# Kernel tuning notes

Measured on AMD Instinct MI355X. Metric: run time of the kernel, lower is better.

## Reference

```python
import jax, jax.numpy as jnp
import numpy as np

# Static config matching init_kwargs
COUT, CIN, K = 64, 64, 3
PAD = K // 2  # padding=1


def setup_inputs() -> dict:
    key = jax.random.key(0)
    k1, k2, k3 = jax.random.split(key, 3)
    B, H, W, FH, FW, SC = 2, 256, 256, 16, 16, 128
    hyper_params = COUT * CIN * K * K  # 36864
    x = jax.random.normal(k1, (B, CIN, H, W), jnp.float32)
    s = jax.random.normal(k2, (B, SC, FH, FW), jnp.float32)
    s2w = jax.random.normal(k3, (hyper_params, SC), jnp.float32) * 0.02
    return {"x": x, "s": s, "s2w": s2w}


def reference(x, s, s2w):
    """HyperPatchConv2d forward: per-patch dynamically generated 3x3 conv.

    x:   [b, c, h, w]   input feature map
    s:   [b, sc, fh, fw] hypernetwork signal (one vector per patch)
    s2w: [P, sc]         signal2weights 1x1 conv (P = out*cin*k*k)
    """
    b, c, h, w = x.shape
    fh, fw = s.shape[-2:]
    ph, pw = h // fh, w // fw          # patch size
    kh, kw = ph + 2 * PAD, pw + 2 * PAD  # unfold window (patch + halo)

    # signal2weights: 1x1 conv -> per-patch flattened conv weight
    wflat = jnp.einsum('pc,bcfg->bfgp', s2w, s)            # [b,fh,fw,P]
    Wdyn = wflat.reshape(b, fh, fw, COUT, CIN, K, K)        # per-patch conv kernels

    # reflect-pad then unfold into overlapping (kh,kw) patches, stride (ph,pw)
    xp = jnp.pad(x, ((0, 0), (0, 0), (PAD, PAD), (PAD, PAD)), mode='reflect')
    idx_h = (jnp.arange(fh) * ph)[:, None] + jnp.arange(kh)[None, :]  # [fh,kh]
    idx_w = (jnp.arange(fw) * pw)[:, None] + jnp.arange(kw)[None, :]  # [fw,kw]
    patches = xp[:, :, idx_h][:, :, :, :, idx_w]            # [b,c,fh,kh,fw,kw]

    # extract KxK sliding windows inside each patch (valid conv, stride 1)
    wi = jnp.arange(ph)[:, None] + jnp.arange(K)[None, :]   # [ph,K]
    wj = jnp.arange(pw)[:, None] + jnp.arange(K)[None, :]   # [pw,K]
    win = patches[:, :, :, wi]                              # [b,c,fh,ph,K,fw,kw]
    win = win[:, :, :, :, :, :, wj]                         # [b,c,fh,ph,K,fw,pw,K]
    win = win.transpose(0, 2, 5, 1, 3, 4, 6, 7)             # [b,fh,fw,c,ph,K,pw,K]

    # per-patch dynamic conv
    out = jnp.einsum('bfgocij,bfgcpiqj->bfgopq', Wdyn, win)  # [b,fh,fw,o,ph,pw]

    # fold: non-overlapping reassembly (stride == patch size)
    return out.transpose(0, 3, 1, 4, 2, 5).reshape(b, COUT, h, w)
```

## Files before the change

### kernel.cpp

```cpp
#include <hip/hip_runtime.h>
#include <hip/hip_bf16.h>


#define C_OUT 64
#define C_IN  64
#define P_TOTAL 36864
#define N_PATCH 512
#define WSTR 72
#define CSTR2 136

typedef __bf16 bf16x8 __attribute__((ext_vector_type(8)));
typedef float  f32x4  __attribute__((ext_vector_type(4)));

__device__ __forceinline__ unsigned short f2bf(float f) {
  unsigned int u = __float_as_uint(f);
  u += 0x7fffu + ((u >> 16) & 1u);
  return (unsigned short)(u >> 16);
}
__device__ __forceinline__ unsigned int pack2(float a, float b) {
  return (unsigned int)f2bf(a) | ((unsigned int)f2bf(b) << 16);
}
__device__ __forceinline__ void gll16(const void* g, void* l) {
  __builtin_amdgcn_global_load_lds(
      (const __attribute__((address_space(1))) void*)g,
      (__attribute__((address_space(3))) void*)l, 16, 0, 0);
}

__global__ __launch_bounds__(256) void prep_ws(
    const float* __restrict__ s, const float* __restrict__ s2w,
    unsigned short* __restrict__ sTg, unsigned short* __restrict__ s2wP) {
  const int bid = blockIdx.x;
  const int t = threadIdx.x;

  if (bid < 32) {
    const int sb = bid >> 4;
    const int g = bid & 15;
    float v[8];
    #pragma unroll
    for (int e = 0; e < 8; ++e)
      v[e] = s[((size_t)(sb * 128 + g * 8 + e)) * 256 + t];
    uint4 o;
    o.x = pack2(v[0], v[1]); o.y = pack2(v[2], v[3]);
    o.z = pack2(v[4], v[5]); o.w = pack2(v[6], v[7]);
    const int ntile = sb * 2 + (t >> 7);
    const int slot = (t & 127) ^ (g & 7);
    *(uint4*)(sTg + ((size_t)(ntile * 2048 + g * 128 + slot)) * 8) = o;
    return;
  }

  const int b3 = bid - 32;
  const int m = b3 * 64 + (t >> 2);
  const int q = t & 3;
  const int j = m & 7;
  const int lane6 = (m >> 3) & 63;
  const int fragidx = m >> 9;
  const int tap = fragidx >> 3;
  const int ksH = (fragidx >> 2) & 1;
  const int mtH = fragidx & 3;
  const int co = mtH * 16 + (lane6 & 15);
  const int ci = ksH * 32 + (lane6 >> 4) * 8 + j;
  const int p = co * 576 + ci * 9 + tap;
  const float* src = s2w + (size_t)p * 128 + q * 32;
  const int mtile = m >> 7;
  const int r128 = m & 127;
  #pragma unroll
  for (int gg = 0; gg < 4; ++gg) {
    const int g = q * 4 + gg;
    const float4 v0 = *(const float4*)(src + gg * 8);
    const float4 v1 = *(const float4*)(src + gg * 8 + 4);
    uint4 o;
    o.x = pack2(v0.x, v0.y); o.y = pack2(v0.z, v0.w);
    o.z = pack2(v1.x, v1.y); o.w = pack2(v1.z, v1.w);
    const int slot = r128 ^ (g & 7);
    *(uint4*)(s2wP + ((size_t)(mtile * 2048 + g * 128 + slot)) * 8) = o;
  }
}

__global__ __launch_bounds__(256) void wgen_plus(
    const float* __restrict__ x,
    const unsigned short* __restrict__ s2wP,
    const unsigned short* __restrict__ sTg,
    unsigned short* __restrict__ xT,
    unsigned short* __restrict__ wout)
{
  __shared__ unsigned short lds[32768];
  const int bid = blockIdx.x;
  const int tid = threadIdx.x;

  if (bid < 512) {
    const int bb = bid >> 8, row = bid & 255;
    unsigned short* xl = lds;
    #pragma unroll
    for (int it = 0; it < 16; ++it) {
      const int ci = it * 4 + (tid >> 6);
      const int px = (tid & 63) * 4;
      const float4 v = *(const float4*)(x + ((size_t)(bb * 64 + ci)) * 65536 + row * 256 + px);
      ushort4 o;
      o.x = f2bf(v.x); o.y = f2bf(v.y); o.z = f2bf(v.z); o.w = f2bf(v.w);
      *(ushort4*)&xl[ci * 260 + px] = o;
    }
    __syncthreads();
    unsigned short* dst = xT + ((size_t)((bb << 16) + (row << 8) + tid)) * 64;
    #pragma unroll
    for (int k8 = 0; k8 < 8; ++k8) {
      const unsigned int w0 = (unsigned int)xl[(k8 * 8 + 0) * 260 + tid] |
                              ((unsigned int)xl[(k8 * 8 + 1) * 260 + tid] << 16);
      const unsigned int w1 = (unsigned int)xl[(k8 * 8 + 2) * 260 + tid] |
                              ((unsigned int)xl[(k8 * 8 + 3) * 260 + tid] << 16);
      const unsigned int w2 = (unsigned int)xl[(k8 * 8 + 4) * 260 + tid] |
                              ((unsigned int)xl[(k8 * 8 + 5) * 260 + tid] << 16);
      const unsigned int w3 = (unsigned int)xl[(k8 * 8 + 6) * 260 + tid] |
                              ((unsigned int)xl[(k8 * 8 + 7) * 260 + tid] << 16);
      *(uint4*)(dst + k8 * 8) = make_uint4(w0, w1, w2, w3);
    }
    return;
  }

  const int bid2 = bid - 512;
  const int n = bid2 / 288;
  const int mt = bid2 - n * 288;
  const int m0 = mt * 128;
  const int n0 = n * 128;
  unsigned short* As = lds;
  unsigned short* Bs = lds + 16384;

  const unsigned short* srcA = s2wP + (size_t)mt * 16384;
  const unsigned short* srcB = sTg + (size_t)n * 16384;
  #pragma unroll
  for (int i = 0; i < 8; ++i)
    gll16(srcA + (size_t)(i * 256 + tid) * 8, As + (i * 256 + tid) * 8);
  #pragma unroll
  for (int i = 0; i < 8; ++i)
    gll16(srcB + (size_t)(i * 256 + tid) * 8, Bs + (i * 256 + tid) * 8);
  __syncthreads();

  const int w = tid >> 6;
  const int lane = tid & 63;
  const int col = lane & 15;
  const int quad = lane >> 4;

  f32x4 acc[2][8] = {};
  #pragma unroll
  for (int ks = 0; ks < 4; ++ks) {
    const int g = ks * 4 + quad;
    const int gb = g * 1024;
    const int gx = (g & 7) * 8;
    bf16x8 afr[2], bfr[8];
    #pragma unroll
    for (int mti = 0; mti < 2; ++mti)
      afr[mti] = *(const bf16x8*)&As[gb + ((((w * 2 + mti) * 16 + col) * 8) ^ gx)];
    #pragma unroll
    for (int nt = 0; nt < 8; ++nt)
      bfr[nt] = *(const bf16x8*)&Bs[gb + (((nt * 16 + col) * 8) ^ gx)];
    #pragma unroll
    for (int mti = 0; mti < 2; ++mti)
      #pragma unroll
      for (int nt = 0; nt < 8; ++nt)
        acc[mti][nt] = __builtin_amdgcn_mfma_f32_16x16x32_bf16(afr[mti], bfr[nt], acc[mti][nt], 0, 0, 0);
  }
  __syncthreads();

  unsigned short* Ct = lds;
  #pragma unroll
  for (int mti = 0; mti < 2; ++mti) {
    const int mloc = (w * 2 + mti) * 16 + quad * 4;
    #pragma unroll
    for (int nt = 0; nt < 8; ++nt) {
      const int pl = nt * 16 + col;
      ushort4 o;
      o.x = f2bf(acc[mti][nt][0]); o.y = f2bf(acc[mti][nt][1]);
      o.z = f2bf(acc[mti][nt][2]); o.w = f2bf(acc[mti][nt][3]);
      *(ushort4*)&Ct[pl * CSTR2 + mloc] = o;
    }
  }
  __syncthreads();
  #pragma unroll
  for (int i = 0; i < 8; ++i) {
    const int chunk = i * 256 + tid;
    const int pl = chunk >> 4;
    const int ii = chunk & 15;
    const uint4 v = *(const uint4*)&Ct[pl * CSTR2 + ii * 8];
    *(uint4*)(wout + (size_t)(n0 + pl) * P_TOTAL + m0 + ii * 8) = v;
  }
}

__global__ __launch_bounds__(512, 2) void conv_kernel(
    const unsigned short* __restrict__ xT,
    const unsigned short* __restrict__ wfrag,
    float* __restrict__ out)
{
  __shared__ unsigned short win[324 * WSTR];
  const int tid = threadIdx.x;
  const int patch = blockIdx.x;
  const int bb = patch >> 8;
  const int fg = patch & 255;
  const int f = fg >> 4, g = fg & 15;
  const int row0 = f * 16, col0 = g * 16;

  for (int chunk = tid; chunk < 2592; chunk += 512) {
    const int cell = chunk >> 3;
    const int j = chunk & 7;
    const int r = cell / 18;
    const int c = cell - r * 18;
    int rr = row0 + r - 1; rr = rr < 0 ? -rr : (rr > 255 ? 510 - rr : rr);
    int cc = col0 + c - 1; cc = cc < 0 ? -cc : (cc > 255 ? 510 - cc : cc);
    *(uint4*)&win[cell * WSTR + j * 8] =
        *(const uint4*)(xT + ((size_t)((bb << 16) + (rr << 8) + cc)) * 64 + j * 8);
  }
  __syncthreads();

  const int wave = tid >> 6;
  const int lane = tid & 63;
  const int t = lane & 15;
  const int quad = lane >> 4;
  const int mh = wave & 1;
  const int rq = wave >> 1;

  f32x4 acc[2][4] = {};
  const bf16x8* wb = (const bf16x8*)(wfrag + (size_t)patch * P_TOTAL);

  #pragma unroll
  for (int tap = 0; tap < 9; ++tap) {
    const int ti = tap / 3;
    const int tj = tap - ti * 3;
    bf16x8 afr[2][2];
    #pragma unroll
    for (int ks = 0; ks < 2; ++ks)
      #pragma unroll
      for (int ml = 0; ml < 2; ++ml)
        afr[ks][ml] = wb[((tap * 2 + ks) * 4 + mh * 2 + ml) * 64 + lane];

    #pragma unroll
    for (int nt = 0; nt < 4; ++nt) {
      const int r = rq * 4 + nt + ti;
      const int c = t + tj;
      const int base = (r * 18 + c) * WSTR + quad * 8;
      #pragma unroll
      for (int ks = 0; ks < 2; ++ks) {
        const bf16x8 bfr = *(const bf16x8*)&win[base + ks * 32];
        acc[0][nt] = __builtin_amdgcn_mfma_f32_16x16x32_bf16(afr[ks][0], bfr, acc[0][nt], 0, 0, 0);
        acc[1][nt] = __builtin_amdgcn_mfma_f32_16x16x32_bf16(afr[ks][1], bfr, acc[1][nt], 0, 0, 0);
      }
    }
  }

  #pragma unroll
  for (int ml = 0; ml < 2; ++ml) {
    #pragma unroll
    for (int nt = 0; nt < 4; ++nt) {
      const int p = row0 + rq * 4 + nt;
      #pragma unroll
      for (int reg = 0; reg < 4; ++reg) {
        const int co = (mh * 2 + ml) * 16 + quad * 4 + reg;
        out[(((size_t)bb * C_OUT + co) << 16) + ((size_t)p << 8) + col0 + t] = acc[ml][nt][reg];
      }
    }
  }
}

extern "C" void kernel_launch(void* const* d_in, const int* in_sizes, int n_in,
                              void* d_out, int out_size, void* d_ws, size_t ws_size,
                              hipStream_t stream) {
  const float* x   = (const float*)d_in[0];
  const float* s   = (const float*)d_in[1];
  const float* s2w = (const float*)d_in[2];
  float* out = (float*)d_out;

  char* ws = (char*)d_ws;
  unsigned short* wbuf = (unsigned short*)(ws);
  unsigned short* sTg  = (unsigned short*)(ws + 37748736);
  unsigned short* xT   = (unsigned short*)(ws + 37879808);
  unsigned short* s2wP = (unsigned short*)(ws + 54657024);

  prep_ws<<<608, 256, 0, stream>>>(s, s2w, sTg, s2wP);
  wgen_plus<<<1664, 256, 0, stream>>>(x, s2wP, sTg, xT, wbuf);
  conv_kernel<<<N_PATCH, 512, 0, stream>>>(xT, wbuf, out);
}
```

Baseline: 129.0 us.

## Fuse signal and weight bf16 packing into the weight-generation GEMM kernel

Removes the separate prep kernel. Each GEMM block now loads fp32 s and s2w tiles directly, converts them to bf16, and writes them swizzled into LDS. This drops one launch and the intermediate workspace write and read. In exchange, s2w tiles are reconverted from fp32 by each of the four n-tile blocks, and the s tile by every m-tile block. That raises global traffic and ALU work, and the async global_load_lds path is no longer used.

```diff
diff --git a/kernel.cpp b/kernel.cpp
--- a/kernel.cpp
+++ b/kernel.cpp
@@ -20,66 +20,11 @@
 __device__ __forceinline__ unsigned int pack2(float a, float b) {
   return (unsigned int)f2bf(a) | ((unsigned int)f2bf(b) << 16);
 }
-__device__ __forceinline__ void gll16(const void* g, void* l) {
-  __builtin_amdgcn_global_load_lds(
-      (const __attribute__((address_space(1))) void*)g,
-      (__attribute__((address_space(3))) void*)l, 16, 0, 0);
-}
-
-__global__ __launch_bounds__(256) void prep_ws(
-    const float* __restrict__ s, const float* __restrict__ s2w,
-    unsigned short* __restrict__ sTg, unsigned short* __restrict__ s2wP) {
-  const int bid = blockIdx.x;
-  const int t = threadIdx.x;
-
-  if (bid < 32) {
-    const int sb = bid >> 4;
-    const int g = bid & 15;
-    float v[8];
-    #pragma unroll
-    for (int e = 0; e < 8; ++e)
-      v[e] = s[((size_t)(sb * 128 + g * 8 + e)) * 256 + t];
-    uint4 o;
-    o.x = pack2(v[0], v[1]); o.y = pack2(v[2], v[3]);
-    o.z = pack2(v[4], v[5]); o.w = pack2(v[6], v[7]);
-    const int ntile = sb * 2 + (t >> 7);
-    const int slot = (t & 127) ^ (g & 7);
-    *(uint4*)(sTg + ((size_t)(ntile * 2048 + g * 128 + slot)) * 8) = o;
-    return;
-  }
-
-  const int b3 = bid - 32;
-  const int m = b3 * 64 + (t >> 2);
-  const int q = t & 3;
-  const int j = m & 7;
-  const int lane6 = (m >> 3) & 63;
-  const int fragidx = m >> 9;
-  const int tap = fragidx >> 3;
-  const int ksH = (fragidx >> 2) & 1;
-  const int mtH = fragidx & 3;
-  const int co = mtH * 16 + (lane6 & 15);
-  const int ci = ksH * 32 + (lane6 >> 4) * 8 + j;
-  const int p = co * 576 + ci * 9 + tap;
-  const float* src = s2w + (size_t)p * 128 + q * 32;
-  const int mtile = m >> 7;
-  const int r128 = m & 127;
-  #pragma unroll
-  for (int gg = 0; gg < 4; ++gg) {
-    const int g = q * 4 + gg;
-    const float4 v0 = *(const float4*)(src + gg * 8);
-    const float4 v1 = *(const float4*)(src + gg * 8 + 4);
-    uint4 o;
-    o.x = pack2(v0.x, v0.y); o.y = pack2(v0.z, v0.w);
-    o.z = pack2(v1.x, v1.y); o.w = pack2(v1.z, v1.w);
-    const int slot = r128 ^ (g & 7);
-    *(uint4*)(s2wP + ((size_t)(mtile * 2048 + g * 128 + slot)) * 8) = o;
-  }
-}
-
-__global__ __launch_bounds__(256) void wgen_plus(
+
+__global__ __launch_bounds__(256) void mega_kernel(
     const float* __restrict__ x,
-    const unsigned short* __restrict__ s2wP,
-    const unsigned short* __restrict__ sTg,
+    const float* __restrict__ s,
+    const float* __restrict__ s2w,
     unsigned short* __restrict__ xT,
     unsigned short* __restrict__ wout)
 {
@@ -124,14 +69,54 @@
   unsigned short* As = lds;
   unsigned short* Bs = lds + 16384;
 
-  const unsigned short* srcA = s2wP + (size_t)mt * 16384;
-  const unsigned short* srcB = sTg + (size_t)n * 16384;
-  #pragma unroll
-  for (int i = 0; i < 8; ++i)
-    gll16(srcA + (size_t)(i * 256 + tid) * 8, As + (i * 256 + tid) * 8);
-  #pragma unroll
-  for (int i = 0; i < 8; ++i)
-    gll16(srcB + (size_t)(i * 256 + tid) * 8, Bs + (i * 256 + tid) * 8);
+  {
+    const int sb = n >> 1;
+    const int fgbase = (n & 1) * 128;
+    #pragma unroll
+    for (int i = 0; i < 8; ++i) {
+      const int task = i * 256 + tid;
+      const int g = task >> 7;
+      const int pl = task & 127;
+      const int fg = fgbase + pl;
+      float v[8];
+      #pragma unroll
+      for (int e = 0; e < 8; ++e)
+        v[e] = s[((size_t)(sb * 128 + g * 8 + e)) * 256 + fg];
+      uint4 o;
+      o.x = pack2(v[0], v[1]); o.y = pack2(v[2], v[3]);
+      o.z = pack2(v[4], v[5]); o.w = pack2(v[6], v[7]);
+      const int slot = pl ^ (g & 7);
+      *(uint4*)&Bs[g * 1024 + slot * 8] = o;
+    }
+  }
+  #pragma unroll
+  for (int it = 0; it < 2; ++it) {
+    const int task = it * 256 + tid;
+    const int row = task >> 2;
+    const int q = task & 3;
+    const int m = m0 + row;
+    const int j = m & 7;
+    const int lane6 = (m >> 3) & 63;
+    const int fragidx = m >> 9;
+    const int tap = fragidx >> 3;
+    const int ksH = (fragidx >> 2) & 1;
+    const int mtH = fragidx & 3;
+    const int co = mtH * 16 + (lane6 & 15);
+    const int ci = ksH * 32 + (lane6 >> 4) * 8 + j;
+    const int p = co * 576 + ci * 9 + tap;
+    const float* src = s2w + (size_t)p * 128 + q * 32;
+    #pragma unroll
+    for (int gg = 0; gg < 4; ++gg) {
+      const int g = q * 4 + gg;
+      const float4 v0 = *(const float4*)(src + gg * 8);
+      const float4 v1 = *(const float4*)(src + gg * 8 + 4);
+      uint4 o;
+      o.x = pack2(v0.x, v0.y); o.y = pack2(v0.z, v0.w);
+      o.z = pack2(v1.x, v1.y); o.w = pack2(v1.z, v1.w);
+      const int slot = row ^ (g & 7);
+      *(uint4*)&As[g * 1024 + slot * 8] = o;
+    }
+  }
   __syncthreads();
 
   const int w = tid >> 6;
@@ -268,11 +253,8 @@
 
   char* ws = (char*)d_ws;
   unsigned short* wbuf = (unsigned short*)(ws);
-  unsigned short* sTg  = (unsigned short*)(ws + 37748736);
-  unsigned short* xT   = (unsigned short*)(ws + 37879808);
-  unsigned short* s2wP = (unsigned short*)(ws + 54657024);
-
-  prep_ws<<<608, 256, 0, stream>>>(s, s2w, sTg, s2wP);
-  wgen_plus<<<1664, 256, 0, stream>>>(x, s2wP, sTg, xT, wbuf);
+  unsigned short* xT   = (unsigned short*)(ws + 37748736);
+
+  mega_kernel<<<1664, 256, 0, stream>>>(x, s, s2w, xT, wbuf);
   conv_kernel<<<N_PATCH, 512, 0, stream>>>(xT, wbuf, out);
 }
```

New measurement: 135.5 us. 1.05x slower.
